# Optimization experiments

Hardware: AMD Instinct MI355X
Metric: run time of the kernel (lower is better)

The kernel has to match this reference:

```python
import jax, jax.numpy as jnp
import numpy as np

B, N, HID, H, M = 4, 16384, 512, 8, 32
D = HID // H  # 64


def setup_inputs() -> dict:
    key = jax.random.key(0)
    ks = jax.random.split(key, 8)
    s = 0.02
    return {
        "x": jax.random.normal(ks[0], (B, N, HID), jnp.float32),
        "wkv": jax.random.normal(ks[1], (2 * HID, HID), jnp.float32) * s,
        "bkv": jnp.zeros((2 * HID,), jnp.float32),
        "wtq": jax.random.normal(ks[2], (H, M, D), jnp.float32) * s,
        "alpha1": jnp.ones((H,), jnp.float32),
        "mix1_w": jax.random.normal(ks[3], (H * M, H * M), jnp.float32) * (1.0 / np.sqrt(H * M)),
        "ln1_w": jnp.ones((D,), jnp.float32),
        "ln1_b": jnp.zeros((D,), jnp.float32),
        "wqkv": jax.random.normal(ks[4], (3 * HID, HID), jnp.float32) * s,
        "wout": jax.random.normal(ks[5], (HID, HID), jnp.float32) * s,
        "bout": jnp.zeros((HID,), jnp.float32),
    }


def _layernorm(x, w, b, eps=1e-5):
    mu = x.mean(-1, keepdims=True)
    var = ((x - mu) ** 2).mean(-1, keepdims=True)
    return (x - mu) * jax.lax.rsqrt(var + eps) * w + b


def reference(x, wkv, bkv, wtq, alpha1, mix1_w, ln1_w, ln1_b, wqkv, wout, bout):
    # key/value projection: [B, N, 2*HID]
    kv = x @ wkv.T + bkv
    xk, xv = jnp.split(kv, 2, axis=-1)
    xk = xk.reshape(B, N, H, D).transpose(0, 2, 1, 3)  # b h n d
    xv = xv.reshape(B, N, H, D).transpose(0, 2, 1, 3)
    # slice scores + 1x1 conv head-mixing over the (H*M) channel dim
    scores = jnp.einsum('hmd,bhnd->bhmn', wtq, xk)
    scores = jnp.einsum('oc,bcn->bon', mix1_w, scores.reshape(B, H * M, N)).reshape(B, H, M, N)
    # softmax over the slice dim M (dim=-2)
    sw = jax.nn.softmax(scores * alpha1[:, None, None], axis=-2)  # b h m n
    # weighted reduction to slice tokens, normalized by total weight per slice
    tok = jnp.einsum('bhmn,bhnd->bhmd', sw, xv)
    tok = tok / (sw.sum(axis=-1, keepdims=True) + 1e-5)
    tok = _layernorm(tok, ln1_w, ln1_b)
    tok = tok.transpose(0, 2, 1, 3).reshape(B, M, HID)  # b m (h d)
    # small inner MHA over the M=32 slice tokens
    qkv = tok @ wqkv.T
    q, k, v = jnp.split(qkv, 3, axis=-1)
    q = q.reshape(B, M, H, D).transpose(0, 2, 1, 3)
    k = k.reshape(B, M, H, D).transpose(0, 2, 1, 3)
    v = v.reshape(B, M, H, D).transpose(0, 2, 1, 3)
    dots = jnp.einsum('bhqd,bhkd->bhqk', q, k) * (D ** -0.5)
    attn = jax.nn.softmax(dots, axis=-1)
    out_tok = jnp.einsum('bhqk,bhkd->bhqd', attn, v)
    # broadcast slice tokens back to the N points via slice weights
    out = jnp.einsum('bhmd,bhmn->bhnd', out_tok, sw)
    out = out.transpose(0, 2, 1, 3).reshape(B, N, HID)
    out = out @ wout.T + bout
    return (out, sw, alpha1[:, None, None], jnp.zeros((H, M), jnp.float32), attn)
```

## Files before the change

kernel.cpp:

```cpp
#include <hip/hip_runtime.h>
#include <hip/hip_bf16.h>

#define B_ 4
#define N_ 16384
#define HID_ 512
#define H_ 8
#define M_ 32
#define D_ 64
#define HM_ 256

typedef __hip_bfloat16 bf16;
typedef __bf16 bf16x8 __attribute__((ext_vector_type(8)));
typedef float f32x4 __attribute__((ext_vector_type(4)));

__device__ __forceinline__ void gl_lds16(const bf16* g, bf16* l) {
    __builtin_amdgcn_global_load_lds(
        (const __attribute__((address_space(1))) void*)g,
        (__attribute__((address_space(3))) void*)l, 16, 0, 0);
}

__device__ __forceinline__ int xcd_swz(int lin, int nwg) {
    return (lin & 7) * (nwg >> 3) + (lin >> 3);
}

__device__ __forceinline__ void mfma_core(
        const bf16* __restrict__ Ag, const bf16* __restrict__ Bg,
        long long arow0, int bcol0, int lda, int ldb, int kiters,
        bf16* As, bf16* Bs, f32x4 acc[4][4]) {
    const int t = threadIdx.x;
    const int l = t & 63, w = t >> 6;
    const int wm = w >> 1, wn = w & 1;
    const int srow = l >> 3;
    const int skel = (l & 7) * 8;
    for (int kt = 0; kt < kiters; ++kt) {
        const int kk = kt * 64;
#pragma unroll
        for (int j = 0; j < 4; ++j) {
            int q = j * 4 + w;
            gl_lds16(Ag + (arow0 + q * 8 + srow) * (long long)lda + kk + skel, As + q * 512);
        }
#pragma unroll
        for (int j = 0; j < 4; ++j) {
            int q = j * 4 + w;
            gl_lds16(Bg + (long long)(bcol0 + q * 8 + srow) * ldb + kk + skel, Bs + q * 512);
        }
        __syncthreads();
#pragma unroll
        for (int ks = 0; ks < 64; ks += 32) {
            bf16x8 af[4], bfr[4];
#pragma unroll
            for (int mf = 0; mf < 4; ++mf)
                af[mf] = *(const bf16x8*)(As + (wm * 64 + mf * 16 + (l & 15)) * 64 + ks + (l >> 4) * 8);
#pragma unroll
            for (int nf = 0; nf < 4; ++nf)
                bfr[nf] = *(const bf16x8*)(Bs + (wn * 64 + nf * 16 + (l & 15)) * 64 + ks + (l >> 4) * 8);
#pragma unroll
            for (int mf = 0; mf < 4; ++mf)
#pragma unroll
                for (int nf = 0; nf < 4; ++nf)
                    acc[mf][nf] = __builtin_amdgcn_mfma_f32_16x16x32_bf16(af[mf], bfr[nf], acc[mf][nf], 0, 0, 0);
        }
        __syncthreads();
    }
}

__global__ __launch_bounds__(256) void k_cast4(const float* __restrict__ s,
        ushort* __restrict__ d) {
    long long i = (long long)blockIdx.x * 256 + threadIdx.x;
    float4 v = reinterpret_cast<const float4*>(s)[i];
    ushort4 o;
    bf16 a0 = __float2bfloat16(v.x), a1 = __float2bfloat16(v.y);
    bf16 a2 = __float2bfloat16(v.z), a3 = __float2bfloat16(v.w);
    o.x = *(ushort*)&a0; o.y = *(ushort*)&a1; o.z = *(ushort*)&a2; o.w = *(ushort*)&a3;
    reinterpret_cast<ushort4*>(d)[i] = o;
}

__global__ __launch_bounds__(256) void k_wfused(const float* __restrict__ mix1,
        const float* __restrict__ wtq, bf16* __restrict__ wf_bt) {
    const int idx = blockIdx.x * 256 + threadIdx.x;
    const int o = idx >> 9, k = idx & 511;
    const int h = k >> 6, dd = k & 63;
    float s = 0.f;
#pragma unroll
    for (int m = 0; m < 32; ++m)
        s += mix1[(long long)o * 256 + h * 32 + m] * wtq[((long long)h * 32 + m) * 64 + dd];
    wf_bt[(long long)o * 512 + k] = __float2bfloat16(s);
}

__global__ __launch_bounds__(256) void k1_mfma(const bf16* __restrict__ xb,
        const bf16* __restrict__ wkvb, const float* __restrict__ bkv,
        bf16* __restrict__ xk, bf16* __restrict__ xv) {
    __shared__ bf16 As[128 * 64], Bs[128 * 64];
    f32x4 acc[4][4];
#pragma unroll
    for (int i = 0; i < 4; ++i)
#pragma unroll
        for (int j = 0; j < 4; ++j) acc[i][j] = (f32x4)(0.0f);
    const int wg = xcd_swz(blockIdx.y * 8 + blockIdx.x, 4096);
    const int bx = wg & 7, by = wg >> 3;
    const long long arow0 = (long long)by * 128;
    const int bcol0 = bx * 128;
    mfma_core(xb, wkvb, arow0, bcol0, 512, 512, 8, As, Bs, acc);
    const int l = threadIdx.x & 63, w = threadIdx.x >> 6;
    const int wm = w >> 1, wn = w & 1;
#pragma unroll
    for (int mf = 0; mf < 4; ++mf) {
#pragma unroll
        for (int nf = 0; nf < 4; ++nf) {
            int col = bcol0 + wn * 64 + nf * 16 + (l & 15);
            float bv = bkv[col];
#pragma unroll
            for (int r = 0; r < 4; ++r) {
                long long row = arow0 + wm * 64 + mf * 16 + (l >> 4) * 4 + r;
                bf16 hv = __float2bfloat16(acc[mf][nf][r] + bv);
                if (col < 512) xk[row * 512 + col] = hv;
                else           xv[row * 512 + (col - 512)] = hv;
            }
        }
    }
}

__global__ __launch_bounds__(256) void k2_mfma(const bf16* __restrict__ xk,
        const bf16* __restrict__ wf_bt, const float* __restrict__ alpha1,
        bf16* __restrict__ sc) {
    __shared__ bf16 As[128 * 64], Bs[128 * 64];
    f32x4 acc[4][4];
#pragma unroll
    for (int i = 0; i < 4; ++i)
#pragma unroll
        for (int j = 0; j < 4; ++j) acc[i][j] = (f32x4)(0.0f);
    const int wg = xcd_swz(blockIdx.y * 2 + blockIdx.x, 1024);
    const int bx = wg & 1, by = wg >> 1;
    const long long arow0 = (long long)by * 128;
    const int bcol0 = bx * 128;
    mfma_core(xk, wf_bt, arow0, bcol0, 512, 512, 8, As, Bs, acc);
    const int l = threadIdx.x & 63, w = threadIdx.x >> 6;
    const int wm = w >> 1, wn = w & 1;
#pragma unroll
    for (int mf = 0; mf < 4; ++mf) {
#pragma unroll
        for (int nf = 0; nf < 4; ++nf) {
            int col = bcol0 + wn * 64 + nf * 16 + (l & 15);
            float al = alpha1[col >> 5];
#pragma unroll
            for (int r = 0; r < 4; ++r) {
                long long row = arow0 + wm * 64 + mf * 16 + (l >> 4) * 4 + r;
                sc[row * 256 + col] = __float2bfloat16(acc[mf][nf][r] * al);
            }
        }
    }
}

__global__ __launch_bounds__(256) void k_softmax(const bf16* __restrict__ sc,
        float* __restrict__ swout, bf16* __restrict__ sw_bt,
        float* __restrict__ part) {
    __shared__ float T[32][257];
    const int t = threadIdx.x;
    const int b = blockIdx.y;
    const int n0 = blockIdx.x * 32;
    const long long rb = (long long)b * N_ + n0;
    for (int i = 0; i < 32; ++i)
        T[i][t] = __bfloat162float(sc[(rb + i) * 256 + t]);
    __syncthreads();
    const int nl = t & 31, h = t >> 5;
    float v[32];
    float mx = -1e30f;
#pragma unroll
    for (int i = 0; i < 32; ++i) { v[i] = T[nl][h * 32 + i]; mx = fmaxf(mx, v[i]); }
    float sum = 0.f;
#pragma unroll
    for (int i = 0; i < 32; ++i) { v[i] = __expf(v[i] - mx); sum += v[i]; }
    float rinv = 1.f / sum;
#pragma unroll
    for (int i = 0; i < 32; ++i) T[nl][h * 32 + i] = v[i] * rinv;
    __syncthreads();
#pragma unroll
    for (int jo = 0; jo < 32; ++jo) {
        int o = h * 32 + jo;
        swout[((long long)b * HM_ + o) * N_ + n0 + nl] = T[nl][o];
    }
    for (int i = 0; i < 32; ++i)
        sw_bt[(rb + i) * 256 + t] = __float2bfloat16(T[i][t]);
    float s = 0.f;
#pragma unroll
    for (int i = 0; i < 32; ++i) s += T[i][t];
    part[((long long)b * 512 + blockIdx.x) * 256 + t] = s;
}

__global__ __launch_bounds__(256) void k_swsum2(const float* __restrict__ part,
        float* __restrict__ swsum) {
    const int b = blockIdx.x, c = threadIdx.x;
    float s = 0.f;
    for (int nb = 0; nb < 512; ++nb)
        s += part[((long long)b * 512 + nb) * 256 + c];
    swsum[b * 256 + c] = s;
}

__global__ __launch_bounds__(256) void k3_tok(const float* __restrict__ sw,
        const bf16* __restrict__ xv, float* __restrict__ tok_part) {
    __shared__ __align__(16) float smem[17408];
    float (*swsT)[36] = reinterpret_cast<float(*)[36]>(smem);
    bf16* xvs = reinterpret_cast<bf16*>(smem + 9216);
    const int t = threadIdx.x;
    const int chunk = blockIdx.x;
    const int bh = blockIdx.y;
    const int n0 = chunk * 256;
    const int b = bh >> 3, h = bh & 7;
    const long long swbase = ((long long)bh * 32) * N_ + n0;
#pragma unroll
    for (int p = 0; p < 8; ++p) {
        float4 v;
        v.x = sw[swbase + (long long)(p * 4 + 0) * N_ + t];
        v.y = sw[swbase + (long long)(p * 4 + 1) * N_ + t];
        v.z = sw[swbase + (long long)(p * 4 + 2) * N_ + t];
        v.w = sw[swbase + (long long)(p * 4 + 3) * N_ + t];
        *reinterpret_cast<float4*>(&swsT[t][p * 4]) = v;
    }
    {
        const uint* xg = reinterpret_cast<const uint*>(xv + ((long long)b * N_ + n0) * 512 + h * 64);
        uint* xls = reinterpret_cast<uint*>(xvs);
#pragma unroll
        for (int p = 0; p < 32; ++p) {
            int idx = p * 256 + t;
            int nl = idx >> 5, prt = idx & 31;
            xls[nl * 32 + prt] = xg[(long long)nl * 256 + prt];
        }
    }
    __syncthreads();
    const int l = t & 63, w = t >> 6;
    const int nlh = l >> 5, mtile = (l >> 3) & 3, dtile = l & 7;
    const int m0 = mtile * 8, d0 = dtile * 8;
    float acc[8][8] = {};
    const int wbase = w * 64;
    for (int i = 0; i < 32; ++i) {
        int nl = wbase + i * 2 + nlh;
        float4 s0 = *reinterpret_cast<const float4*>(&swsT[nl][m0]);
        float4 s1 = *reinterpret_cast<const float4*>(&swsT[nl][m0 + 4]);
        uint4 xi = *reinterpret_cast<const uint4*>(&xvs[nl * 64 + d0]);
        float xvf[8];
        xvf[0] = __uint_as_float(xi.x << 16); xvf[1] = __uint_as_float(xi.x & 0xffff0000u);
        xvf[2] = __uint_as_float(xi.y << 16); xvf[3] = __uint_as_float(xi.y & 0xffff0000u);
        xvf[4] = __uint_as_float(xi.z << 16); xvf[5] = __uint_as_float(xi.z & 0xffff0000u);
        xvf[6] = __uint_as_float(xi.w << 16); xvf[7] = __uint_as_float(xi.w & 0xffff0000u);
        float sm[8] = {s0.x, s0.y, s0.z, s0.w, s1.x, s1.y, s1.z, s1.w};
#pragma unroll
        for (int mi = 0; mi < 8; ++mi)
#pragma unroll
            for (int di = 0; di < 8; ++di)
                acc[mi][di] += sm[mi] * xvf[di];
    }
    __syncthreads();
    float* red = smem;
    float* rb = red + (w * 2 + nlh) * 2048;
#pragma unroll
    for (int mi = 0; mi < 8; ++mi) {
        float4 lo = {acc[mi][0], acc[mi][1], acc[mi][2], acc[mi][3]};
        float4 hi = {acc[mi][4], acc[mi][5], acc[mi][6], acc[mi][7]};
        *reinterpret_cast<float4*>(&rb[(m0 + mi) * 64 + d0]) = lo;
        *reinterpret_cast<float4*>(&rb[(m0 + mi) * 64 + d0 + 4]) = hi;
    }
    __syncthreads();
#pragma unroll
    for (int pp = 0; pp < 2; ++pp) {
        int idx4 = pp * 1024 + t * 4;
        float4 s = {0.f, 0.f, 0.f, 0.f};
#pragma unroll
        for (int r = 0; r < 8; ++r) {
            float4 v = *reinterpret_cast<const float4*>(&red[r * 2048 + idx4]);
            s.x += v.x; s.y += v.y; s.z += v.z; s.w += v.w;
        }
        *reinterpret_cast<float4*>(&tok_part[((long long)bh * 64 + chunk) * 2048 + idx4]) = s;
    }
}

__global__ __launch_bounds__(64) void k4a_ln(const float* __restrict__ tok_part,
        const float* __restrict__ swsum, const float* __restrict__ ln_w,
        const float* __restrict__ ln_b, float* __restrict__ tok_ln) {
    const int bid = blockIdx.x;
    const int bh = bid >> 5, m = bid & 31;
    const int d = threadIdx.x;
    float s = 0.f;
    for (int ch = 0; ch < 64; ++ch)
        s += tok_part[(((long long)bh * 64 + ch) * 32 + m) * 64 + d];
    float tokv = s / (swsum[bid] + 1e-5f);
    float mu = tokv;
#pragma unroll
    for (int mk = 32; mk >= 1; mk >>= 1) mu += __shfl_xor(mu, mk, 64);
    mu *= (1.f / 64.f);
    float df = tokv - mu;
    float var = df * df;
#pragma unroll
    for (int mk = 32; mk >= 1; mk >>= 1) var += __shfl_xor(var, mk, 64);
    var *= (1.f / 64.f);
    float y = df * rsqrtf(var + 1e-5f) * ln_w[d] + ln_b[d];
    const int b = bh >> 3, h = bh & 7;
    tok_ln[((long long)b * 32 + m) * 512 + h * 64 + d] = y;
}

__global__ __launch_bounds__(256) void k_wqT(const float* __restrict__ wq,
        float* __restrict__ wqT) {
    __shared__ float tile[32][33];
    const int k0 = blockIdx.x * 32;
    const int j0 = blockIdx.y * 32;
    const int tx = threadIdx.x & 31, ty = threadIdx.x >> 5;
#pragma unroll
    for (int r = 0; r < 32; r += 8)
        tile[ty + r][tx] = wq[(long long)(j0 + ty + r) * 512 + k0 + tx];
    __syncthreads();
#pragma unroll
    for (int r = 0; r < 32; r += 8)
        wqT[(long long)(k0 + ty + r) * 1536 + j0 + tx] = tile[tx][ty + r];
}

__global__ __launch_bounds__(256) void k4b_qkv(const float* __restrict__ tok_ln,
        const float* __restrict__ wqT, float* __restrict__ qkv) {
    const int j = (blockIdx.x % 6) * 256 + threadIdx.x;
    const int r0 = (blockIdx.x / 6) * 4;
    float a0 = 0, a1 = 0, a2 = 0, a3 = 0;
    for (int k = 0; k < 512; ++k) {
        float wv = wqT[(long long)k * 1536 + j];
        a0 += tok_ln[(r0 + 0) * 512 + k] * wv;
        a1 += tok_ln[(r0 + 1) * 512 + k] * wv;
        a2 += tok_ln[(r0 + 2) * 512 + k] * wv;
        a3 += tok_ln[(r0 + 3) * 512 + k] * wv;
    }
    qkv[(long long)(r0 + 0) * 1536 + j] = a0;
    qkv[(long long)(r0 + 1) * 1536 + j] = a1;
    qkv[(long long)(r0 + 2) * 1536 + j] = a2;
    qkv[(long long)(r0 + 3) * 1536 + j] = a3;
}

__global__ __launch_bounds__(256) void k4c_attn(const float* __restrict__ qkv,
        float* __restrict__ out_tok, float* __restrict__ attn_out) {
    __shared__ float qsT[64][33], ksT[64][33], vsT[64][33];
    __shared__ float att[32][33];
    __shared__ float rinv[32];
    const int t = threadIdx.x;
    const int bid = blockIdx.x;
    const int b = bid >> 3, h = bid & 7;
#pragma unroll
    for (int i = 0; i < 8; ++i) {
        int idx = i * 256 + t;
        int mi = idx >> 6, dd = idx & 63;
        long long base = ((long long)b * 32 + mi) * 1536 + h * 64 + dd;
        qsT[dd][mi] = qkv[base];
        ksT[dd][mi] = qkv[base + 512];
        vsT[dd][mi] = qkv[base + 1024];
    }
    __syncthreads();
#pragma unroll
    for (int i = 0; i < 4; ++i) {
        int idx = i * 256 + t;
        int qi = idx >> 5, ki = idx & 31;
        float s = 0.f;
#pragma unroll
        for (int dd = 0; dd < 64; ++dd) s += qsT[dd][qi] * ksT[dd][ki];
        att[qi][ki] = s * 0.125f;
    }
    __syncthreads();
    if (t < 32) {
        float mx = -1e30f;
        for (int k = 0; k < 32; ++k) mx = fmaxf(mx, att[t][k]);
        float sum = 0.f;
        for (int k = 0; k < 32; ++k) { float e = __expf(att[t][k] - mx); att[t][k] = e; sum += e; }
        rinv[t] = 1.f / sum;
    }
    __syncthreads();
#pragma unroll
    for (int i = 0; i < 4; ++i) {
        int idx = i * 256 + t;
        int qi = idx >> 5, ki = idx & 31;
        float a = att[qi][ki] * rinv[qi];
        att[qi][ki] = a;
        attn_out[(long long)bid * 1024 + qi * 32 + ki] = a;
    }
    __syncthreads();
#pragma unroll
    for (int i = 0; i < 8; ++i) {
        int idx = i * 256 + t;
        int qi = idx >> 6, dd = idx & 63;
        float s = 0.f;
#pragma unroll
        for (int ki = 0; ki < 32; ++ki) s += att[qi][ki] * vsT[dd][ki];
        out_tok[((long long)bid * 32 + qi) * 64 + dd] = s;
    }
}

__global__ __launch_bounds__(256) void k5_w2(const float* __restrict__ wout,
        const float* __restrict__ out_tok, bf16* __restrict__ W2) {
    const int bid = blockIdx.x;
    const int b = bid >> 9, o = bid & 511;
    const int t = threadIdx.x;
    const int h = t >> 5, m = t & 31;
    float s = 0.f;
#pragma unroll
    for (int dd = 0; dd < 64; ++dd)
        s += wout[(long long)o * 512 + h * 64 + dd]
           * out_tok[(((long long)b * 8 + h) * 32 + m) * 64 + dd];
    W2[(long long)bid * 256 + t] = __float2bfloat16(s);
}

__global__ __launch_bounds__(256) void k6_mfma(const bf16* __restrict__ sw_bt,
        const bf16* __restrict__ W2, const float* __restrict__ bout,
        float* __restrict__ out) {
    __shared__ bf16 As[128 * 64], Bs[128 * 64];
    f32x4 acc[4][4];
#pragma unroll
    for (int i = 0; i < 4; ++i)
#pragma unroll
        for (int j = 0; j < 4; ++j) acc[i][j] = (f32x4)(0.0f);
    const int wg = xcd_swz((blockIdx.z * 128 + blockIdx.y) * 4 + blockIdx.x, 2048);
    const int bx = wg & 3, by = (wg >> 2) & 127, bz = wg >> 9;
    const long long arow0 = (long long)by * 128;
    const int bcol0 = bx * 128;
    mfma_core(sw_bt + (long long)bz * N_ * 256, W2 + (long long)bz * 512 * 256,
              arow0, bcol0, 256, 256, 4, As, Bs, acc);
    const int l = threadIdx.x & 63, w = threadIdx.x >> 6;
    const int wm = w >> 1, wn = w & 1;
#pragma unroll
    for (int mf = 0; mf < 4; ++mf) {
#pragma unroll
        for (int nf = 0; nf < 4; ++nf) {
            int col = bcol0 + wn * 64 + nf * 16 + (l & 15);
            float bv = bout[col];
#pragma unroll
            for (int r = 0; r < 4; ++r) {
                long long row = arow0 + wm * 64 + mf * 16 + (l >> 4) * 4 + r;
                out[((long long)bz * N_ + row) * 512 + col] = acc[mf][nf][r] + bv;
            }
        }
    }
}

__global__ void k_misc(const float* __restrict__ alpha1,
        float* __restrict__ outA, float* __restrict__ outZ) {
    int t = threadIdx.x;
    if (t < 8) outA[t] = alpha1[t];
    outZ[t] = 0.f;
}

extern "C" void kernel_launch(void* const* d_in, const int* in_sizes, int n_in,
                              void* d_out, int out_size, void* d_ws, size_t ws_size,
                              hipStream_t stream) {
    const float* x      = (const float*)d_in[0];
    const float* wkv    = (const float*)d_in[1];
    const float* bkv    = (const float*)d_in[2];
    const float* wtq    = (const float*)d_in[3];
    const float* alpha1 = (const float*)d_in[4];
    const float* mix1_w = (const float*)d_in[5];
    const float* ln1_w  = (const float*)d_in[6];
    const float* ln1_b  = (const float*)d_in[7];
    const float* wqkv   = (const float*)d_in[8];
    const float* wout   = (const float*)d_in[9];
    const float* bout   = (const float*)d_in[10];

    float* out    = (float*)d_out;
    float* swout  = out + 33554432LL;
    float* alphaO = out + 50331648LL;
    float* zerosO = out + 50331656LL;
    float* attnO  = out + 50331912LL;

    char* ws = (char*)d_ws;
    bf16*  xb        = (bf16*)(ws);
    bf16*  sc        = (bf16*)(ws);
    float* wqkvT     = (float*)(ws);
    bf16*  sw_bt     = (bf16*)(ws + 33554432LL);
    bf16*  xk        = (bf16*)(ws + 67108864LL);
    float* swsum_prt = (float*)(ws + 67108864LL);
    bf16*  xv        = (bf16*)(ws + 134217728LL);
    float* tok_part  = (float*)(ws + 201326592LL);
    float* swsum     = (float*)(ws + 218103808LL);
    float* tok_ln    = (float*)(ws + 218107904LL);
    float* qkv       = (float*)(ws + 218370048LL);
    float* out_tok   = (float*)(ws + 219156480LL);
    bf16*  W2b       = (bf16*)(ws + 219418624LL);
    bf16*  wkvb      = (bf16*)(ws + 220467200LL);
    bf16*  wf_bt     = (bf16*)(ws + 221515776LL);

    k_cast4<<<32768, 256, 0, stream>>>(x, (ushort*)xb);
    k_cast4<<<512, 256, 0, stream>>>(wkv, (ushort*)wkvb);
    k_wfused<<<512, 256, 0, stream>>>(mix1_w, wtq, wf_bt);
    k1_mfma<<<dim3(8, 512), 256, 0, stream>>>(xb, wkvb, bkv, xk, xv);
    k2_mfma<<<dim3(2, 512), 256, 0, stream>>>(xk, wf_bt, alpha1, sc);
    k_softmax<<<dim3(512, 4), 256, 0, stream>>>(sc, swout, sw_bt, swsum_prt);
    k_wqT<<<dim3(16, 48), 256, 0, stream>>>(wqkv, wqkvT);
    k_swsum2<<<4, 256, 0, stream>>>(swsum_prt, swsum);
    k3_tok<<<dim3(64, 32), 256, 0, stream>>>(swout, xv, tok_part);
    k4a_ln<<<1024, 64, 0, stream>>>(tok_part, swsum, ln1_w, ln1_b, tok_ln);
    k4b_qkv<<<192, 256, 0, stream>>>(tok_ln, wqkvT, qkv);
    k4c_attn<<<32, 256, 0, stream>>>(qkv, out_tok, attnO);
    k5_w2<<<2048, 256, 0, stream>>>(wout, out_tok, W2b);
    k6_mfma<<<dim3(4, 128, 4), 256, 0, stream>>>(sw_bt, W2b, bout, out);
    k_misc<<<1, 256, 0, stream>>>(alpha1, alphaO, zerosO);
}
```

Before: 375.3 us.

## Double-buffer MFMA GEMMs, swizzle LDS, fuse x cast into k1, vectorize epilogues

Replaces the single-buffered GEMM core with a double-buffered pipeline that prefetches the next K tile while computing the current one. It also XOR-swizzles the LDS layout to avoid bank conflicts. The x fp32-to-bf16 cast kernel is removed; k1 now loads fp32 x directly, converts it in registers and writes it to LDS, saving a full pass over x. Epilogues of k1/k2 go through LDS to emit packed 16-byte bf16 stores instead of scattered 2-byte stores. The cost is doubled LDS use (64KB per block), which may reduce occupancy.

```diff
diff --git a/kernel.cpp b/kernel.cpp
--- a/kernel.cpp
+++ b/kernel.cpp
@@ -23,44 +23,76 @@
     return (lin & 7) * (nwg >> 3) + (lin >> 3);
 }
 
-__device__ __forceinline__ void mfma_core(
-        const bf16* __restrict__ Ag, const bf16* __restrict__ Bg,
-        long long arow0, int bcol0, int lda, int ldb, int kiters,
-        bf16* As, bf16* Bs, f32x4 acc[4][4]) {
-    const int t = threadIdx.x;
+__device__ __forceinline__ uint bpk(float lo, float hi) {
+    bf16 a = __float2bfloat16(lo), b = __float2bfloat16(hi);
+    return (uint)(*(ushort*)&a) | ((uint)(*(ushort*)&b) << 16);
+}
+
+__device__ __forceinline__ void stage_tile(const bf16* __restrict__ G, long long r0,
+        int kk, int ld, bf16* lds, int t) {
     const int l = t & 63, w = t >> 6;
-    const int wm = w >> 1, wn = w & 1;
     const int srow = l >> 3;
-    const int skel = (l & 7) * 8;
-    for (int kt = 0; kt < kiters; ++kt) {
-        const int kk = kt * 64;
-#pragma unroll
-        for (int j = 0; j < 4; ++j) {
-            int q = j * 4 + w;
-            gl_lds16(Ag + (arow0 + q * 8 + srow) * (long long)lda + kk + skel, As + q * 512);
-        }
-#pragma unroll
-        for (int j = 0; j < 4; ++j) {
-            int q = j * 4 + w;
-            gl_lds16(Bg + (long long)(bcol0 + q * 8 + srow) * ldb + kk + skel, Bs + q * 512);
-        }
+    const int skel = ((l & 7) ^ srow) * 8;
+#pragma unroll
+    for (int j = 0; j < 4; ++j) {
+        int q = j * 4 + w;
+        gl_lds16(G + (r0 + q * 8 + srow) * (long long)ld + kk + skel, lds + q * 512);
+    }
+}
+
+__device__ __forceinline__ void mfma_tile(const bf16* Ab, const bf16* Bb,
+        int l, int wm, int wn, f32x4 acc[4][4]) {
+    const int l15 = l & 15;
+    const int xsw = (l & 7) * 8;
+    const int kq = (l >> 4) * 8;
+#pragma unroll
+    for (int ks = 0; ks < 64; ks += 32) {
+        const int ko = (ks + kq) ^ xsw;
+        bf16x8 af[4], bfr[4];
+#pragma unroll
+        for (int mf = 0; mf < 4; ++mf)
+            af[mf] = *(const bf16x8*)(Ab + (wm * 64 + mf * 16 + l15) * 64 + ko);
+#pragma unroll
+        for (int nf = 0; nf < 4; ++nf)
+            bfr[nf] = *(const bf16x8*)(Bb + (wn * 64 + nf * 16 + l15) * 64 + ko);
+#pragma unroll
+        for (int mf = 0; mf < 4; ++mf)
+#pragma unroll
+            for (int nf = 0; nf < 4; ++nf)
+                acc[mf][nf] = __builtin_amdgcn_mfma_f32_16x16x32_bf16(af[mf], bfr[nf], acc[mf][nf], 0, 0, 0);
+    }
+}
+
+__device__ __forceinline__ void awrite(bf16* Ab, int ar, int kh, const float4* a) {
+    const int rx = (ar & 7) * 8;
+#pragma unroll
+    for (int j = 0; j < 4; ++j) {
+        uint4 p;
+        p.x = bpk(a[2 * j].x, a[2 * j].y);
+        p.y = bpk(a[2 * j].z, a[2 * j].w);
+        p.z = bpk(a[2 * j + 1].x, a[2 * j + 1].y);
+        p.w = bpk(a[2 * j + 1].z, a[2 * j + 1].w);
+        *reinterpret_cast<uint4*>(Ab + ar * 64 + ((kh * 32 + j * 8) ^ rx)) = p;
+    }
+}
+
+__device__ __forceinline__ void gemm_dbuf(const bf16* __restrict__ Ag,
+        const bf16* __restrict__ Bg, long long arow0, int bcol0, int lda, int ldb,
+        int nt, bf16 (*As)[8192], bf16 (*Bs)[8192], f32x4 acc[4][4]) {
+    const int t = threadIdx.x;
+    const int l = t & 63, w = t >> 6, wm = w >> 1, wn = w & 1;
+    stage_tile(Ag, arow0, 0, lda, As[0], t);
+    stage_tile(Bg, bcol0, 0, ldb, Bs[0], t);
+    __syncthreads();
+    int cur = 0;
+    for (int kt = 0; kt < nt; ++kt) {
+        if (kt + 1 < nt) {
+            stage_tile(Ag, arow0, (kt + 1) * 64, lda, As[cur ^ 1], t);
+            stage_tile(Bg, bcol0, (kt + 1) * 64, ldb, Bs[cur ^ 1], t);
+        }
+        mfma_tile(As[cur], Bs[cur], l, wm, wn, acc);
         __syncthreads();
-#pragma unroll
-        for (int ks = 0; ks < 64; ks += 32) {
-            bf16x8 af[4], bfr[4];
-#pragma unroll
-            for (int mf = 0; mf < 4; ++mf)
-                af[mf] = *(const bf16x8*)(As + (wm * 64 + mf * 16 + (l & 15)) * 64 + ks + (l >> 4) * 8);
-#pragma unroll
-            for (int nf = 0; nf < 4; ++nf)
-                bfr[nf] = *(const bf16x8*)(Bs + (wn * 64 + nf * 16 + (l & 15)) * 64 + ks + (l >> 4) * 8);
-#pragma unroll
-            for (int mf = 0; mf < 4; ++mf)
-#pragma unroll
-                for (int nf = 0; nf < 4; ++nf)
-                    acc[mf][nf] = __builtin_amdgcn_mfma_f32_16x16x32_bf16(af[mf], bfr[nf], acc[mf][nf], 0, 0, 0);
-        }
-        __syncthreads();
+        cur ^= 1;
     }
 }
 
@@ -87,10 +119,10 @@
     wf_bt[(long long)o * 512 + k] = __float2bfloat16(s);
 }
 
-__global__ __launch_bounds__(256) void k1_mfma(const bf16* __restrict__ xb,
+__global__ __launch_bounds__(256) void k1_mfma(const float* __restrict__ x,
         const bf16* __restrict__ wkvb, const float* __restrict__ bkv,
         bf16* __restrict__ xk, bf16* __restrict__ xv) {
-    __shared__ bf16 As[128 * 64], Bs[128 * 64];
+    __shared__ bf16 As[2][8192], Bs[2][8192];
     f32x4 acc[4][4];
 #pragma unroll
     for (int i = 0; i < 4; ++i)
@@ -100,30 +132,65 @@
     const int bx = wg & 7, by = wg >> 3;
     const long long arow0 = (long long)by * 128;
     const int bcol0 = bx * 128;
-    mfma_core(xb, wkvb, arow0, bcol0, 512, 512, 8, As, Bs, acc);
-    const int l = threadIdx.x & 63, w = threadIdx.x >> 6;
-    const int wm = w >> 1, wn = w & 1;
+    const int t = threadIdx.x;
+    const int l = t & 63, w = t >> 6, wm = w >> 1, wn = w & 1;
+    const int ar = t >> 1, kh = t & 1;
+    const float* xrow = x + (arow0 + ar) * 512 + kh * 32;
+
+    float4 a[8];
+#pragma unroll
+    for (int j = 0; j < 8; ++j) a[j] = *(const float4*)(xrow + j * 4);
+    stage_tile(wkvb, bcol0, 0, 512, Bs[0], t);
+    awrite(As[0], ar, kh, a);
+    __syncthreads();
+    int cur = 0;
+    for (int kt = 0; kt < 8; ++kt) {
+        if (kt < 7) {
+#pragma unroll
+            for (int j = 0; j < 8; ++j) a[j] = *(const float4*)(xrow + (kt + 1) * 64 + j * 4);
+            stage_tile(wkvb, bcol0, (kt + 1) * 64, 512, Bs[cur ^ 1], t);
+        }
+        mfma_tile(As[cur], Bs[cur], l, wm, wn, acc);
+        if (kt < 7) awrite(As[cur ^ 1], ar, kh, a);
+        __syncthreads();
+        cur ^= 1;
+    }
+    float* eps = (float*)&As[0][0];
+    float* my = eps + w * 1024;
+    const int l15 = l & 15, lq = l >> 4;
+    float bv[4];
+#pragma unroll
+    for (int nf = 0; nf < 4; ++nf) bv[nf] = bkv[bcol0 + wn * 64 + nf * 16 + l15];
 #pragma unroll
     for (int mf = 0; mf < 4; ++mf) {
 #pragma unroll
-        for (int nf = 0; nf < 4; ++nf) {
-            int col = bcol0 + wn * 64 + nf * 16 + (l & 15);
-            float bv = bkv[col];
-#pragma unroll
-            for (int r = 0; r < 4; ++r) {
-                long long row = arow0 + wm * 64 + mf * 16 + (l >> 4) * 4 + r;
-                bf16 hv = __float2bfloat16(acc[mf][nf][r] + bv);
-                if (col < 512) xk[row * 512 + col] = hv;
-                else           xv[row * 512 + (col - 512)] = hv;
-            }
-        }
+        for (int nf = 0; nf < 4; ++nf)
+#pragma unroll
+            for (int r = 0; r < 4; ++r)
+                my[(lq * 4 + r) * 64 + nf * 16 + l15] = acc[mf][nf][r] + bv[nf];
+        __syncthreads();
+#pragma unroll
+        for (int p = 0; p < 2; ++p) {
+            int lrow = p * 8 + (l >> 3);
+            const float* src = my + lrow * 64 + (l & 7) * 8;
+            float4 v0 = *(const float4*)src, v1 = *(const float4*)(src + 4);
+            uint4 pk;
+            pk.x = bpk(v0.x, v0.y); pk.y = bpk(v0.z, v0.w);
+            pk.z = bpk(v1.x, v1.y); pk.w = bpk(v1.z, v1.w);
+            long long grow = arow0 + wm * 64 + mf * 16 + lrow;
+            int gcol = bcol0 + wn * 64 + (l & 7) * 8;
+            bf16* dst = (gcol < 512) ? (xk + grow * 512 + gcol)
+                                     : (xv + grow * 512 + gcol - 512);
+            *reinterpret_cast<uint4*>(dst) = pk;
+        }
+        __syncthreads();
     }
 }
 
 __global__ __launch_bounds__(256) void k2_mfma(const bf16* __restrict__ xk,
         const bf16* __restrict__ wf_bt, const float* __restrict__ alpha1,
         bf16* __restrict__ sc) {
-    __shared__ bf16 As[128 * 64], Bs[128 * 64];
+    __shared__ bf16 As[2][8192], Bs[2][8192];
     f32x4 acc[4][4];
 #pragma unroll
     for (int i = 0; i < 4; ++i)
@@ -133,21 +200,36 @@
     const int bx = wg & 1, by = wg >> 1;
     const long long arow0 = (long long)by * 128;
     const int bcol0 = bx * 128;
-    mfma_core(xk, wf_bt, arow0, bcol0, 512, 512, 8, As, Bs, acc);
-    const int l = threadIdx.x & 63, w = threadIdx.x >> 6;
-    const int wm = w >> 1, wn = w & 1;
+    gemm_dbuf(xk, wf_bt, arow0, bcol0, 512, 512, 8, As, Bs, acc);
+    const int t = threadIdx.x;
+    const int l = t & 63, w = t >> 6, wm = w >> 1, wn = w & 1;
+    float* eps = (float*)&As[0][0];
+    float* my = eps + w * 1024;
+    const int l15 = l & 15, lq = l >> 4;
+    float al[4];
+#pragma unroll
+    for (int nf = 0; nf < 4; ++nf) al[nf] = alpha1[(bcol0 + wn * 64 + nf * 16 + l15) >> 5];
 #pragma unroll
     for (int mf = 0; mf < 4; ++mf) {
 #pragma unroll
-        for (int nf = 0; nf < 4; ++nf) {
-            int col = bcol0 + wn * 64 + nf * 16 + (l & 15);
-            float al = alpha1[col >> 5];
-#pragma unroll
-            for (int r = 0; r < 4; ++r) {
-                long long row = arow0 + wm * 64 + mf * 16 + (l >> 4) * 4 + r;
-                sc[row * 256 + col] = __float2bfloat16(acc[mf][nf][r] * al);
-            }
-        }
+        for (int nf = 0; nf < 4; ++nf)
+#pragma unroll
+            for (int r = 0; r < 4; ++r)
+                my[(lq * 4 + r) * 64 + nf * 16 + l15] = acc[mf][nf][r] * al[nf];
+        __syncthreads();
+#pragma unroll
+        for (int p = 0; p < 2; ++p) {
+            int lrow = p * 8 + (l >> 3);
+            const float* src = my + lrow * 64 + (l & 7) * 8;
+            float4 v0 = *(const float4*)src, v1 = *(const float4*)(src + 4);
+            uint4 pk;
+            pk.x = bpk(v0.x, v0.y); pk.y = bpk(v0.z, v0.w);
+            pk.z = bpk(v1.x, v1.y); pk.w = bpk(v1.z, v1.w);
+            long long grow = arow0 + wm * 64 + mf * 16 + lrow;
+            int gcol = bcol0 + wn * 64 + (l & 7) * 8;
+            *reinterpret_cast<uint4*>(sc + grow * 256 + gcol) = pk;
+        }
+        __syncthreads();
     }
 }
 
@@ -403,7 +485,7 @@
 __global__ __launch_bounds__(256) void k6_mfma(const bf16* __restrict__ sw_bt,
         const bf16* __restrict__ W2, const float* __restrict__ bout,
         float* __restrict__ out) {
-    __shared__ bf16 As[128 * 64], Bs[128 * 64];
+    __shared__ bf16 As[2][8192], Bs[2][8192];
     f32x4 acc[4][4];
 #pragma unroll
     for (int i = 0; i < 4; ++i)
@@ -413,7 +495,7 @@
     const int bx = wg & 3, by = (wg >> 2) & 127, bz = wg >> 9;
     const long long arow0 = (long long)by * 128;
     const int bcol0 = bx * 128;
-    mfma_core(sw_bt + (long long)bz * N_ * 256, W2 + (long long)bz * 512 * 256,
+    gemm_dbuf(sw_bt + (long long)bz * N_ * 256, W2 + (long long)bz * 512 * 256,
               arow0, bcol0, 256, 256, 4, As, Bs, acc);
     const int l = threadIdx.x & 63, w = threadIdx.x >> 6;
     const int wm = w >> 1, wn = w & 1;
@@ -461,7 +543,6 @@
     float* attnO  = out + 50331912LL;
 
     char* ws = (char*)d_ws;
-    bf16*  xb        = (bf16*)(ws);
     bf16*  sc        = (bf16*)(ws);
     float* wqkvT     = (float*)(ws);
     bf16*  sw_bt     = (bf16*)(ws + 33554432LL);
@@ -477,10 +558,9 @@
     bf16*  wkvb      = (bf16*)(ws + 220467200LL);
     bf16*  wf_bt     = (bf16*)(ws + 221515776LL);
 
-    k_cast4<<<32768, 256, 0, stream>>>(x, (ushort*)xb);
     k_cast4<<<512, 256, 0, stream>>>(wkv, (ushort*)wkvb);
     k_wfused<<<512, 256, 0, stream>>>(mix1_w, wtq, wf_bt);
-    k1_mfma<<<dim3(8, 512), 256, 0, stream>>>(xb, wkvb, bkv, xk, xv);
+    k1_mfma<<<dim3(8, 512), 256, 0, stream>>>(x, wkvb, bkv, xk, xv);
     k2_mfma<<<dim3(2, 512), 256, 0, stream>>>(xk, wf_bt, alpha1, sc);
     k_softmax<<<dim3(512, 4), 256, 0, stream>>>(sc, swout, sw_bt, swsum_prt);
     k_wqT<<<dim3(16, 48), 256, 0, stream>>>(wqkv, wqkvT);
```

Result: slower. 464.3 us (+23.7%).

## Fuse fp32-to-bf16 cast of x into KV projection GEMM with double-buffered weights

Applied to the files above, without the earlier changes.

Drops the separate cast kernel for x. The KV projection GEMM now reads fp32 x straight into registers and converts it to bf16 in place before the MFMAs. The weight tile goes through double-buffered, XOR-swizzled LDS with a prefetch, and the epilogue stages results through LDS so bf16 output is written in 16-byte vector stores. The goal is to avoid writing and re-reading a 64MB bf16 copy of x and to cut the kernel launch. In exchange, each of the 8 column blocks re-reads fp32 x (twice the bytes of bf16) without LDS sharing, and register pressure rises.

```diff
diff --git a/kernel.cpp b/kernel.cpp
--- a/kernel.cpp
+++ b/kernel.cpp
@@ -23,6 +23,35 @@
     return (lin & 7) * (nwg >> 3) + (lin >> 3);
 }
 
+__device__ __forceinline__ uint bpk(float lo, float hi) {
+    bf16 a = __float2bfloat16(lo), b = __float2bfloat16(hi);
+    return (uint)(*(ushort*)&a) | ((uint)(*(ushort*)&b) << 16);
+}
+
+__device__ __forceinline__ void stage_tile_sw(const bf16* __restrict__ G, long long r0,
+        int kk, int ld, bf16* lds, int t) {
+    const int l = t & 63, w = t >> 6;
+    const int srow = l >> 3;
+    const int skel = ((l & 7) ^ srow) * 8;
+#pragma unroll
+    for (int j = 0; j < 4; ++j) {
+        int q = j * 4 + w;
+        gl_lds16(G + (r0 + q * 8 + srow) * (long long)ld + kk + skel, lds + q * 512);
+    }
+}
+
+__device__ __forceinline__ void stage_tile_lin(const bf16* __restrict__ G, long long r0,
+        int kk, int ld, bf16* lds, int t) {
+    const int l = t & 63, w = t >> 6;
+    const int srow = l >> 3;
+    const int skel = (l & 7) * 8;
+#pragma unroll
+    for (int j = 0; j < 4; ++j) {
+        int q = j * 4 + w;
+        gl_lds16(G + (r0 + q * 8 + srow) * (long long)ld + kk + skel, lds + q * 512);
+    }
+}
+
 __device__ __forceinline__ void mfma_core(
         const bf16* __restrict__ Ag, const bf16* __restrict__ Bg,
         long long arow0, int bcol0, int lda, int ldb, int kiters,
@@ -30,20 +59,10 @@
     const int t = threadIdx.x;
     const int l = t & 63, w = t >> 6;
     const int wm = w >> 1, wn = w & 1;
-    const int srow = l >> 3;
-    const int skel = (l & 7) * 8;
     for (int kt = 0; kt < kiters; ++kt) {
         const int kk = kt * 64;
-#pragma unroll
-        for (int j = 0; j < 4; ++j) {
-            int q = j * 4 + w;
-            gl_lds16(Ag + (arow0 + q * 8 + srow) * (long long)lda + kk + skel, As + q * 512);
-        }
-#pragma unroll
-        for (int j = 0; j < 4; ++j) {
-            int q = j * 4 + w;
-            gl_lds16(Bg + (long long)(bcol0 + q * 8 + srow) * ldb + kk + skel, Bs + q * 512);
-        }
+        stage_tile_lin(Ag, arow0, kk, lda, As, t);
+        stage_tile_lin(Bg, bcol0, kk, ldb, Bs, t);
         __syncthreads();
 #pragma unroll
         for (int ks = 0; ks < 64; ks += 32) {
@@ -62,6 +81,14 @@
         }
         __syncthreads();
     }
+}
+
+__device__ __forceinline__ bf16x8 cvt8(const float* p) {
+    float4 v0 = *(const float4*)p, v1 = *(const float4*)(p + 4);
+    union { uint4 u4; bf16x8 h; } c;
+    c.u4.x = bpk(v0.x, v0.y); c.u4.y = bpk(v0.z, v0.w);
+    c.u4.z = bpk(v1.x, v1.y); c.u4.w = bpk(v1.z, v1.w);
+    return c.h;
 }
 
 __global__ __launch_bounds__(256) void k_cast4(const float* __restrict__ s,
@@ -87,10 +114,10 @@
     wf_bt[(long long)o * 512 + k] = __float2bfloat16(s);
 }
 
-__global__ __launch_bounds__(256) void k1_mfma(const bf16* __restrict__ xb,
+__global__ __launch_bounds__(256) void k1_mfma(const float* __restrict__ x,
         const bf16* __restrict__ wkvb, const float* __restrict__ bkv,
         bf16* __restrict__ xk, bf16* __restrict__ xv) {
-    __shared__ bf16 As[128 * 64], Bs[128 * 64];
+    __shared__ bf16 Bs[2][8192];
     f32x4 acc[4][4];
 #pragma unroll
     for (int i = 0; i < 4; ++i)
@@ -100,23 +127,86 @@
     const int bx = wg & 7, by = wg >> 3;
     const long long arow0 = (long long)by * 128;
     const int bcol0 = bx * 128;
-    mfma_core(xb, wkvb, arow0, bcol0, 512, 512, 8, As, Bs, acc);
-    const int l = threadIdx.x & 63, w = threadIdx.x >> 6;
-    const int wm = w >> 1, wn = w & 1;
+    const int t = threadIdx.x;
+    const int l = t & 63, w = t >> 6, wm = w >> 1, wn = w & 1;
+    const int l15 = l & 15;
+    const int xsw = (l & 7) * 8;
+    const int kq = (l >> 4) * 8;
+
+    stage_tile_sw(wkvb, bcol0, 0, 512, Bs[0], t);
+    asm volatile("s_waitcnt vmcnt(0)" ::: "memory");
+    __builtin_amdgcn_s_barrier();
+
+    int cur = 0;
+    for (int kt = 0; kt < 8; ++kt) {
+        float4 araw[4][4];
+#pragma unroll
+        for (int mf = 0; mf < 4; ++mf) {
+            const float* ap = x + (arow0 + wm * 64 + mf * 16 + l15) * 512LL + kt * 64 + kq;
+            araw[mf][0] = *(const float4*)ap;
+            araw[mf][1] = *(const float4*)(ap + 4);
+            araw[mf][2] = *(const float4*)(ap + 32);
+            araw[mf][3] = *(const float4*)(ap + 36);
+        }
+        if (kt < 7) stage_tile_sw(wkvb, bcol0, (kt + 1) * 64, 512, Bs[cur ^ 1], t);
+        bf16x8 bfr[2][4];
+#pragma unroll
+        for (int s = 0; s < 2; ++s) {
+            const int ko = (s * 32 + kq) ^ xsw;
+#pragma unroll
+            for (int nf = 0; nf < 4; ++nf)
+                bfr[s][nf] = *(const bf16x8*)(Bs[cur] + (wn * 64 + nf * 16 + l15) * 64 + ko);
+        }
+        __builtin_amdgcn_s_setprio(1);
+#pragma unroll
+        for (int s = 0; s < 2; ++s) {
+#pragma unroll
+            for (int mf = 0; mf < 4; ++mf) {
+                union { uint4 u4; bf16x8 h; } c;
+                c.u4.x = bpk(araw[mf][2 * s].x, araw[mf][2 * s].y);
+                c.u4.y = bpk(araw[mf][2 * s].z, araw[mf][2 * s].w);
+                c.u4.z = bpk(araw[mf][2 * s + 1].x, araw[mf][2 * s + 1].y);
+                c.u4.w = bpk(araw[mf][2 * s + 1].z, araw[mf][2 * s + 1].w);
+#pragma unroll
+                for (int nf = 0; nf < 4; ++nf)
+                    acc[mf][nf] = __builtin_amdgcn_mfma_f32_16x16x32_bf16(c.h, bfr[s][nf], acc[mf][nf], 0, 0, 0);
+            }
+        }
+        __builtin_amdgcn_s_setprio(0);
+        asm volatile("s_waitcnt vmcnt(0)" ::: "memory");
+        __builtin_amdgcn_s_barrier();
+        cur ^= 1;
+    }
+
+    float* eps = (float*)&Bs[0][0];
+    float* my = eps + w * 1024;
+    const int lq = l >> 4;
+    float bv[4];
+#pragma unroll
+    for (int nf = 0; nf < 4; ++nf) bv[nf] = bkv[bcol0 + wn * 64 + nf * 16 + l15];
 #pragma unroll
     for (int mf = 0; mf < 4; ++mf) {
 #pragma unroll
-        for (int nf = 0; nf < 4; ++nf) {
-            int col = bcol0 + wn * 64 + nf * 16 + (l & 15);
-            float bv = bkv[col];
-#pragma unroll
-            for (int r = 0; r < 4; ++r) {
-                long long row = arow0 + wm * 64 + mf * 16 + (l >> 4) * 4 + r;
-                bf16 hv = __float2bfloat16(acc[mf][nf][r] + bv);
-                if (col < 512) xk[row * 512 + col] = hv;
-                else           xv[row * 512 + (col - 512)] = hv;
-            }
-        }
+        for (int nf = 0; nf < 4; ++nf)
+#pragma unroll
+            for (int r = 0; r < 4; ++r)
+                my[(lq * 4 + r) * 64 + nf * 16 + l15] = acc[mf][nf][r] + bv[nf];
+        __syncthreads();
+#pragma unroll
+        for (int p = 0; p < 2; ++p) {
+            int lrow = p * 8 + (l >> 3);
+            const float* src = my + lrow * 64 + (l & 7) * 8;
+            float4 v0 = *(const float4*)src, v1 = *(const float4*)(src + 4);
+            uint4 pk;
+            pk.x = bpk(v0.x, v0.y); pk.y = bpk(v0.z, v0.w);
+            pk.z = bpk(v1.x, v1.y); pk.w = bpk(v1.z, v1.w);
+            long long grow = arow0 + wm * 64 + mf * 16 + lrow;
+            int gcol = bcol0 + wn * 64 + (l & 7) * 8;
+            bf16* dst = (gcol < 512) ? (xk + grow * 512 + gcol)
+                                     : (xv + grow * 512 + gcol - 512);
+            *reinterpret_cast<uint4*>(dst) = pk;
+        }
+        __syncthreads();
     }
 }
 
@@ -461,7 +551,6 @@
     float* attnO  = out + 50331912LL;
 
     char* ws = (char*)d_ws;
-    bf16*  xb        = (bf16*)(ws);
     bf16*  sc        = (bf16*)(ws);
     float* wqkvT     = (float*)(ws);
     bf16*  sw_bt     = (bf16*)(ws + 33554432LL);
@@ -477,10 +566,9 @@
     bf16*  wkvb      = (bf16*)(ws + 220467200LL);
     bf16*  wf_bt     = (bf16*)(ws + 221515776LL);
 
-    k_cast4<<<32768, 256, 0, stream>>>(x, (ushort*)xb);
     k_cast4<<<512, 256, 0, stream>>>(wkv, (ushort*)wkvb);
     k_wfused<<<512, 256, 0, stream>>>(mix1_w, wtq, wf_bt);
-    k1_mfma<<<dim3(8, 512), 256, 0, stream>>>(xb, wkvb, bkv, xk, xv);
+    k1_mfma<<<dim3(8, 512), 256, 0, stream>>>(x, wkvb, bkv, xk, xv);
     k2_mfma<<<dim3(2, 512), 256, 0, stream>>>(xk, wf_bt, alpha1, sc);
     k_softmax<<<dim3(512, 4), 256, 0, stream>>>(sc, swout, sw_bt, swsum_prt);
     k_wqT<<<dim3(16, 48), 256, 0, stream>>>(wqkv, wqkvT);
```

After: 546.6 us. 1.46x slower.

## Fold key projection into score weights and fuse both GEMMs into one

Applied to the files above, without the earlier changes.

Because the score path is linear in xk, the fused mix/query weight is premultiplied with the key half of wkv (alpha folded in) on the device, along with a matching bias. A single GEMM over 768 output columns then produces xv and the scores directly. This removes the full xk intermediate write and read and the second GEMM launch, at the cost of small weight-prep kernels. Scores are now computed from bf16 x against a bf16 composite weight rather than from rounded xk, which changes rounding slightly.

```diff
diff --git a/kernel.cpp b/kernel.cpp
--- a/kernel.cpp
+++ b/kernel.cpp
@@ -23,6 +23,18 @@
     return (lin & 7) * (nwg >> 3) + (lin >> 3);
 }
 
+__device__ __forceinline__ void stage_tile_lin(const bf16* __restrict__ G, long long r0,
+        int kk, int ld, bf16* lds, int t) {
+    const int l = t & 63, w = t >> 6;
+    const int srow = l >> 3;
+    const int skel = (l & 7) * 8;
+#pragma unroll
+    for (int j = 0; j < 4; ++j) {
+        int q = j * 4 + w;
+        gl_lds16(G + (r0 + q * 8 + srow) * (long long)ld + kk + skel, lds + q * 512);
+    }
+}
+
 __device__ __forceinline__ void mfma_core(
         const bf16* __restrict__ Ag, const bf16* __restrict__ Bg,
         long long arow0, int bcol0, int lda, int ldb, int kiters,
@@ -30,20 +42,10 @@
     const int t = threadIdx.x;
     const int l = t & 63, w = t >> 6;
     const int wm = w >> 1, wn = w & 1;
-    const int srow = l >> 3;
-    const int skel = (l & 7) * 8;
     for (int kt = 0; kt < kiters; ++kt) {
         const int kk = kt * 64;
-#pragma unroll
-        for (int j = 0; j < 4; ++j) {
-            int q = j * 4 + w;
-            gl_lds16(Ag + (arow0 + q * 8 + srow) * (long long)lda + kk + skel, As + q * 512);
-        }
-#pragma unroll
-        for (int j = 0; j < 4; ++j) {
-            int q = j * 4 + w;
-            gl_lds16(Bg + (long long)(bcol0 + q * 8 + srow) * ldb + kk + skel, Bs + q * 512);
-        }
+        stage_tile_lin(Ag, arow0, kk, lda, As, t);
+        stage_tile_lin(Bg, bcol0, kk, ldb, Bs, t);
         __syncthreads();
 #pragma unroll
         for (int ks = 0; ks < 64; ks += 32) {
@@ -76,7 +78,7 @@
 }
 
 __global__ __launch_bounds__(256) void k_wfused(const float* __restrict__ mix1,
-        const float* __restrict__ wtq, bf16* __restrict__ wf_bt) {
+        const float* __restrict__ wtq, float* __restrict__ wf) {
     const int idx = blockIdx.x * 256 + threadIdx.x;
     const int o = idx >> 9, k = idx & 511;
     const int h = k >> 6, dd = k & 63;
@@ -84,23 +86,57 @@
 #pragma unroll
     for (int m = 0; m < 32; ++m)
         s += mix1[(long long)o * 256 + h * 32 + m] * wtq[((long long)h * 32 + m) * 64 + dd];
-    wf_bt[(long long)o * 512 + k] = __float2bfloat16(s);
-}
-
-__global__ __launch_bounds__(256) void k1_mfma(const bf16* __restrict__ xb,
-        const bf16* __restrict__ wkvb, const float* __restrict__ bkv,
-        bf16* __restrict__ xk, bf16* __restrict__ xv) {
+    wf[(long long)o * 512 + k] = s;
+}
+
+__global__ __launch_bounds__(256) void k_wsc(const float* __restrict__ wf,
+        const float* __restrict__ wkv, const float* __restrict__ bkv,
+        const float* __restrict__ alpha1, bf16* __restrict__ wv_sc,
+        float* __restrict__ bias768) {
+    __shared__ float wfrow[512];
+    __shared__ float red[256];
+    const int o = blockIdx.x, t = threadIdx.x;
+    wfrow[t] = wf[(long long)o * 512 + t];
+    wfrow[t + 256] = wf[(long long)o * 512 + 256 + t];
+    __syncthreads();
+    const float al = alpha1[o >> 5];
+    float a0 = 0.f, a1 = 0.f;
+    for (int c = 0; c < 512; ++c) {
+        float wv = wfrow[c];
+        a0 += wv * wkv[(long long)c * 512 + t];
+        a1 += wv * wkv[(long long)c * 512 + t + 256];
+    }
+    wv_sc[(long long)(512 + o) * 512 + t] = __float2bfloat16(a0 * al);
+    wv_sc[(long long)(512 + o) * 512 + t + 256] = __float2bfloat16(a1 * al);
+    float p = wfrow[t] * bkv[t] + wfrow[t + 256] * bkv[t + 256];
+    red[t] = p; __syncthreads();
+    for (int s = 128; s >= 1; s >>= 1) {
+        if (t < s) red[t] += red[t + s];
+        __syncthreads();
+    }
+    if (t == 0) bias768[512 + o] = red[0] * al;
+}
+
+__global__ __launch_bounds__(256) void k_prep(const float* __restrict__ bkv,
+        float* __restrict__ bias768) {
+    int j = blockIdx.x * 256 + threadIdx.x;
+    bias768[j] = bkv[512 + j];
+}
+
+__global__ __launch_bounds__(256) void k12_mfma(const bf16* __restrict__ xb,
+        const bf16* __restrict__ wv_sc, const float* __restrict__ bias768,
+        bf16* __restrict__ xv, bf16* __restrict__ sc) {
     __shared__ bf16 As[128 * 64], Bs[128 * 64];
     f32x4 acc[4][4];
 #pragma unroll
     for (int i = 0; i < 4; ++i)
 #pragma unroll
         for (int j = 0; j < 4; ++j) acc[i][j] = (f32x4)(0.0f);
-    const int wg = xcd_swz(blockIdx.y * 8 + blockIdx.x, 4096);
-    const int bx = wg & 7, by = wg >> 3;
+    const int wg = xcd_swz(blockIdx.y * 6 + blockIdx.x, 3072);
+    const int bx = wg % 6, by = wg / 6;
     const long long arow0 = (long long)by * 128;
     const int bcol0 = bx * 128;
-    mfma_core(xb, wkvb, arow0, bcol0, 512, 512, 8, As, Bs, acc);
+    mfma_core(xb, wv_sc, arow0, bcol0, 512, 512, 8, As, Bs, acc);
     const int l = threadIdx.x & 63, w = threadIdx.x >> 6;
     const int wm = w >> 1, wn = w & 1;
 #pragma unroll
@@ -108,44 +144,13 @@
 #pragma unroll
         for (int nf = 0; nf < 4; ++nf) {
             int col = bcol0 + wn * 64 + nf * 16 + (l & 15);
-            float bv = bkv[col];
+            float bv = bias768[col];
 #pragma unroll
             for (int r = 0; r < 4; ++r) {
                 long long row = arow0 + wm * 64 + mf * 16 + (l >> 4) * 4 + r;
                 bf16 hv = __float2bfloat16(acc[mf][nf][r] + bv);
-                if (col < 512) xk[row * 512 + col] = hv;
-                else           xv[row * 512 + (col - 512)] = hv;
-            }
-        }
-    }
-}
-
-__global__ __launch_bounds__(256) void k2_mfma(const bf16* __restrict__ xk,
-        const bf16* __restrict__ wf_bt, const float* __restrict__ alpha1,
-        bf16* __restrict__ sc) {
-    __shared__ bf16 As[128 * 64], Bs[128 * 64];
-    f32x4 acc[4][4];
-#pragma unroll
-    for (int i = 0; i < 4; ++i)
-#pragma unroll
-        for (int j = 0; j < 4; ++j) acc[i][j] = (f32x4)(0.0f);
-    const int wg = xcd_swz(blockIdx.y * 2 + blockIdx.x, 1024);
-    const int bx = wg & 1, by = wg >> 1;
-    const long long arow0 = (long long)by * 128;
-    const int bcol0 = bx * 128;
-    mfma_core(xk, wf_bt, arow0, bcol0, 512, 512, 8, As, Bs, acc);
-    const int l = threadIdx.x & 63, w = threadIdx.x >> 6;
-    const int wm = w >> 1, wn = w & 1;
-#pragma unroll
-    for (int mf = 0; mf < 4; ++mf) {
-#pragma unroll
-        for (int nf = 0; nf < 4; ++nf) {
-            int col = bcol0 + wn * 64 + nf * 16 + (l & 15);
-            float al = alpha1[col >> 5];
-#pragma unroll
-            for (int r = 0; r < 4; ++r) {
-                long long row = arow0 + wm * 64 + mf * 16 + (l >> 4) * 4 + r;
-                sc[row * 256 + col] = __float2bfloat16(acc[mf][nf][r] * al);
+                if (col < 512) xv[row * 512 + col] = hv;
+                else           sc[row * 256 + (col - 512)] = hv;
             }
         }
     }
@@ -462,11 +467,11 @@
 
     char* ws = (char*)d_ws;
     bf16*  xb        = (bf16*)(ws);
-    bf16*  sc        = (bf16*)(ws);
     float* wqkvT     = (float*)(ws);
-    bf16*  sw_bt     = (bf16*)(ws + 33554432LL);
-    bf16*  xk        = (bf16*)(ws + 67108864LL);
-    float* swsum_prt = (float*)(ws + 67108864LL);
+    float* swsum_prt = (float*)(ws + 33554432LL);
+    float* wf_f32    = (float*)(ws + 35651584LL);
+    bf16*  sc        = (bf16*)(ws + 67108864LL);
+    bf16*  sw_bt     = (bf16*)(ws + 100663296LL);
     bf16*  xv        = (bf16*)(ws + 134217728LL);
     float* tok_part  = (float*)(ws + 201326592LL);
     float* swsum     = (float*)(ws + 218103808LL);
@@ -474,14 +479,15 @@
     float* qkv       = (float*)(ws + 218370048LL);
     float* out_tok   = (float*)(ws + 219156480LL);
     bf16*  W2b       = (bf16*)(ws + 219418624LL);
-    bf16*  wkvb      = (bf16*)(ws + 220467200LL);
-    bf16*  wf_bt     = (bf16*)(ws + 221515776LL);
-
+    bf16*  wv_sc     = (bf16*)(ws + 220467200LL);
+    float* bias768   = (float*)(ws + 221253632LL);
+
+    k_cast4<<<256, 256, 0, stream>>>(wkv + 262144, (ushort*)wv_sc);
+    k_wfused<<<512, 256, 0, stream>>>(mix1_w, wtq, wf_f32);
+    k_wsc<<<256, 256, 0, stream>>>(wf_f32, wkv, bkv, alpha1, wv_sc, bias768);
+    k_prep<<<2, 256, 0, stream>>>(bkv, bias768);
     k_cast4<<<32768, 256, 0, stream>>>(x, (ushort*)xb);
-    k_cast4<<<512, 256, 0, stream>>>(wkv, (ushort*)wkvb);
-    k_wfused<<<512, 256, 0, stream>>>(mix1_w, wtq, wf_bt);
-    k1_mfma<<<dim3(8, 512), 256, 0, stream>>>(xb, wkvb, bkv, xk, xv);
-    k2_mfma<<<dim3(2, 512), 256, 0, stream>>>(xk, wf_bt, alpha1, sc);
+    k12_mfma<<<dim3(6, 512), 256, 0, stream>>>(xb, wv_sc, bias768, xv, sc);
     k_softmax<<<dim3(512, 4), 256, 0, stream>>>(sc, swout, sw_bt, swsum_prt);
     k_wqT<<<dim3(16, 48), 256, 0, stream>>>(wqkv, wqkvT);
     k_swsum2<<<4, 256, 0, stream>>>(swsum_prt, swsum);
```

Result: faster. 364.1 us (-3.0%).
